# Kernel optimization log

Hardware: AMD Instinct MI355X
Metric: run time of the kernel (lower is better)

The kernel has to match this reference:

```python
import jax, jax.numpy as jnp
import numpy as np

N_NODES = 50000
N_EDGES = 800000
D = 128          # node / edge / u feature dim
OUT = 128
N_GRAPHS = 64
IN1 = 4 * D      # 512
IN2 = D + OUT + D  # 384


def setup_inputs() -> dict:
    key = jax.random.key(0)
    ks = jax.random.split(key, 10)
    x = jax.random.normal(ks[0], (N_NODES, D), dtype=jnp.float32)
    edge_index = jax.random.randint(ks[1], (2, N_EDGES), 0, N_NODES, dtype=jnp.int64)
    edge_attr = jax.random.normal(ks[2], (N_EDGES, D), dtype=jnp.float32)
    u = jax.random.normal(ks[3], (N_GRAPHS, D), dtype=jnp.float32)
    batch = jnp.sort(jax.random.randint(ks[4], (N_NODES,), 0, N_GRAPHS, dtype=jnp.int64))
    # MLP params (Linear: y = x @ W.T + b), kaiming-ish scale
    W1 = jax.random.normal(ks[5], (OUT, IN1), dtype=jnp.float32) / np.sqrt(IN1)
    b1 = jnp.zeros((OUT,), dtype=jnp.float32)
    W2 = jax.random.normal(ks[6], (OUT, IN2), dtype=jnp.float32) / np.sqrt(IN2)
    b2 = jnp.zeros((OUT,), dtype=jnp.float32)
    return {"x": x, "edge_index": edge_index, "edge_attr": edge_attr,
            "u": u, "batch": batch, "W1": W1, "b1": b1, "W2": W2, "b2": b2}


def reference(x, edge_index, edge_attr, u, batch, W1, b1, W2, b2):
    src, dst = edge_index[0], edge_index[1]
    source_features = x[src]                  # [E, D]
    dest_features = x[dst]                    # [E, D]
    u_edge = u[batch[dst]]                    # [E, D]
    edge_input = jnp.concatenate([dest_features, source_features, edge_attr, u_edge], axis=1)  # [E, IN1]
    edge_messages = jax.nn.relu(edge_input @ W1.T + b1)  # [E, OUT]
    aggregated = jax.ops.segment_sum(edge_messages, dst, num_segments=x.shape[0])  # [N, OUT]
    u_expanded = u[batch]                     # [N, D]
    node_input = jnp.concatenate([x, aggregated, u_expanded], axis=1)  # [N, IN2]
    return jax.nn.relu(node_input @ W2.T + b2)  # [N, OUT]
```

## Files before the change

kernel.cpp:

```cpp
#include <hip/hip_runtime.h>
#include <stdint.h>

#define NNODES 50000
#define NEDGES 800000
#define DIM 128
#define IN1 512
#define IN2 384
#define NSB 196

typedef __attribute__((ext_vector_type(8))) short bf16x8;
typedef __attribute__((ext_vector_type(8))) unsigned short u16x8;
typedef __attribute__((ext_vector_type(4))) float f32x4;
typedef __attribute__((ext_vector_type(4))) uint32_t u32x4;

__device__ __forceinline__ unsigned short f2bf(float f) {
  union { float f; uint32_t u; } v; v.f = f;
  return (unsigned short)((v.u + 0x7FFFu + ((v.u >> 16) & 1u)) >> 16);
}
__device__ __forceinline__ float bf2f(unsigned short u) {
  union { uint32_t u; float f; } v; v.u = ((uint32_t)u) << 16;
  return v.f;
}
__device__ __forceinline__ uint32_t cvtpk(float lo, float hi) {
  uint32_t r;
  asm volatile("v_cvt_pk_bf16_f32 %0, %1, %2" : "=v"(r) : "v"(lo), "v"(hi));
  return r;
}

__device__ __forceinline__ void cvt8(const float* __restrict__ p, unsigned short* dst, int sidx) {
  float4 f0 = *(const float4*)(p);
  float4 f1 = *(const float4*)(p + 4);
  u16x8 o;
  o[0] = f2bf(f0.x); o[1] = f2bf(f0.y); o[2] = f2bf(f0.z); o[3] = f2bf(f0.w);
  o[4] = f2bf(f1.x); o[5] = f2bf(f1.y); o[6] = f2bf(f1.z); o[7] = f2bf(f1.w);
  *(u16x8*)(dst + sidx) = o;
}

__device__ __forceinline__ void mfma128(const unsigned short* As, const unsigned short* Bs,
                                        f32x4 acc[4][4], int wm, int wn, int l) {
#pragma unroll
  for (int kk = 0; kk < 4; ++kk) {
    bf16x8 a[4], b[4];
#pragma unroll
    for (int mi = 0; mi < 4; ++mi) {
      int row = wm * 64 + mi * 16 + (l & 15);
      int idx = (row * 128 + kk * 32 + (l >> 4) * 8) ^ ((row & 7) << 3);
      a[mi] = *(const bf16x8*)(As + idx);
    }
#pragma unroll
    for (int ni = 0; ni < 4; ++ni) {
      int nrow = wn * 64 + ni * 16 + (l & 15);
      int idx = (nrow * 128 + kk * 32 + (l >> 4) * 8) ^ ((nrow & 7) << 3);
      b[ni] = *(const bf16x8*)(Bs + idx);
    }
#pragma unroll
    for (int mi = 0; mi < 4; ++mi)
#pragma unroll
      for (int ni = 0; ni < 4; ++ni)
        acc[mi][ni] = __builtin_amdgcn_mfma_f32_16x16x32_bf16(a[mi], b[ni], acc[mi][ni], 0, 0, 0);
  }
}

__global__ void p0_kernel(const float* __restrict__ u,
                          const float* __restrict__ W1, const float* __restrict__ b1,
                          const float* __restrict__ W2, const float* __restrict__ b2,
                          float* __restrict__ Ud, float* __restrict__ Uc) {
  int g = blockIdx.x, c = threadIdx.x;
  const float* ur = u + (size_t)g * DIM;
  const float* w1 = W1 + (size_t)c * IN1 + 384;
  const float* w2 = W2 + (size_t)c * IN2 + 256;
  float s1 = b1[c], s2 = b2[c];
  for (int k = 0; k < DIM; ++k) { float uv = ur[k]; s1 += uv * w1[k]; s2 += uv * w2[k]; }
  Ud[g * DIM + c] = s1;
  Uc[g * DIM + c] = s2;
}

__global__ void wconv_kernel(const float* __restrict__ W1, const float* __restrict__ W2,
                             unsigned short* __restrict__ Wt) {
  int t = blockIdx.x * 256 + threadIdx.x;
  int tile = t >> 14, rem = t & 16383, n = rem >> 7, k = rem & 127;
  float v = (tile < 3) ? W1[(size_t)n * IN1 + tile * 128 + k]
                       : W2[(size_t)n * IN2 + (tile - 3) * 128 + k];
  int lin = ((n * 128 + (k & ~7)) ^ ((n & 7) << 3)) | (k & 7);
  Wt[tile * 16384 + lin] = f2bf(v);
}

__global__ __launch_bounds__(256, 2) void p1_kernel(
    const float* __restrict__ x, const int* __restrict__ batch,
    const unsigned short* __restrict__ Wt,
    const float* __restrict__ Ud, const float* __restrict__ Uc,
    unsigned short* __restrict__ Xad, unsigned short* __restrict__ Xb,
    unsigned short* __restrict__ Yx) {
  __shared__ __align__(16) unsigned short As[128 * 128];
  __shared__ __align__(16) unsigned short Bs[128 * 128];
  const int t = threadIdx.x, l = t & 63, w = t >> 6, wm = w >> 1, wn = w & 1;
  const int n0 = blockIdx.x * 128, r = t >> 1, h = t & 1;
  const int swz = (r & 7) << 3;
  {
    int n = n0 + r; if (n >= NNODES) n = NNODES - 1;
    const float* rowp = x + (size_t)n * DIM + h * 64;
#pragma unroll
    for (int i = 0; i < 8; ++i) cvt8(rowp + i * 8, As, (r * 128 + h * 64 + i * 8) ^ swz);
  }
#pragma unroll
  for (int p = 0; p < 3; ++p) {
    __syncthreads();
    {
      const u16x8* wsrc = (const u16x8*)(Wt + (size_t)((p == 2) ? 3 : p) * 16384);
      u16x8* bdst = (u16x8*)Bs;
#pragma unroll
      for (int i = 0; i < 8; ++i) bdst[t + i * 256] = wsrc[t + i * 256];
    }
    __syncthreads();
    f32x4 acc[4][4] = {};
    mfma128(As, Bs, acc, wm, wn, l);
#pragma unroll
    for (int mi = 0; mi < 4; ++mi)
#pragma unroll
      for (int rr = 0; rr < 4; ++rr) {
        int m = wm * 64 + mi * 16 + (l >> 4) * 4 + rr;
        int n = n0 + m;
        if (n < NNODES) {
          int g = batch[n];
#pragma unroll
          for (int ni = 0; ni < 4; ++ni) {
            int col = wn * 64 + ni * 16 + (l & 15);
            float v = acc[mi][ni][rr];
            if (p == 0)      Xad[(size_t)n * DIM + col] = f2bf(v + Ud[g * DIM + col]);
            else if (p == 1) Xb [(size_t)n * DIM + col] = f2bf(v);
            else             Yx [(size_t)n * DIM + col] = f2bf(v + Uc[g * DIM + col]);
          }
        }
      }
  }
}

__global__ void hist_kernel(const int* __restrict__ dstI, int* __restrict__ count) {
  int e = blockIdx.x * 256 + threadIdx.x;
  if (e < NEDGES) atomicAdd(&count[dstI[e]], 1);
}

__global__ void scan1_kernel(const int* __restrict__ count, int* __restrict__ bsum) {
  __shared__ int ws[4];
  int i = blockIdx.x * 256 + threadIdx.x;
  int v = (i < NNODES) ? count[i] : 0;
  int l = threadIdx.x & 63;
#pragma unroll
  for (int off = 32; off > 0; off >>= 1) v += __shfl_down(v, off);
  if (l == 0) ws[threadIdx.x >> 6] = v;
  __syncthreads();
  if (threadIdx.x == 0) bsum[blockIdx.x] = ws[0] + ws[1] + ws[2] + ws[3];
}

__global__ void scan2_kernel(const int* __restrict__ bsum, int* __restrict__ bpre) {
  __shared__ int s[256];
  int i = threadIdx.x;
  int v = (i < NSB) ? bsum[i] : 0;
  s[i] = v; __syncthreads();
  for (int off = 1; off < 256; off <<= 1) {
    int u = (i >= off) ? s[i - off] : 0;
    __syncthreads();
    s[i] += u;
    __syncthreads();
  }
  if (i < NSB) bpre[i] = s[i] - v;
}

__global__ void scan3_kernel(const int* __restrict__ count, const int* __restrict__ bpre,
                             int* __restrict__ rowptr) {
  __shared__ int s[256];
  int b = blockIdx.x, i = threadIdx.x, g = b * 256 + i;
  int v = (g < NNODES) ? count[g] : 0;
  s[i] = v; __syncthreads();
  for (int off = 1; off < 256; off <<= 1) {
    int u = (i >= off) ? s[i - off] : 0;
    __syncthreads();
    s[i] += u;
    __syncthreads();
  }
  if (g < NNODES) rowptr[g] = bpre[b] + s[i] - v;
}

__global__ void scatter_kernel(const int* __restrict__ srcI, const int* __restrict__ dstI,
                               int* __restrict__ rowptr, uint64_t* __restrict__ esd) {
  int e = blockIdx.x * 256 + threadIdx.x;
  if (e < NEDGES) {
    int d = dstI[e], s = srcI[e];
    int pos = atomicAdd(&rowptr[d], 1);
    esd[pos] = ((uint64_t)(uint32_t)e << 32) | ((uint32_t)s << 16) | (uint32_t)d;
  }
}

__global__ __launch_bounds__(512, 6) void edge2_kernel(
    const float* __restrict__ ea, const uint64_t* __restrict__ esd,
    const unsigned short* __restrict__ W1cs,
    const unsigned short* __restrict__ Xad, const unsigned short* __restrict__ Xb,
    float* __restrict__ agg) {
  __shared__ __align__(16) unsigned short smem[24576];
  __shared__ int dlds[64];
  __shared__ int slds[64];
  unsigned short* As = smem;
  unsigned short* Bs = smem + 8192;
  unsigned short* Xbs = smem;
  float* Ms = (float*)(smem + 8192);

  const int t = threadIdx.x, l = t & 63, w = t >> 6;
  const int wm = w >> 2, wn = w & 3;
  int bid = blockIdx.x;
  const int nwg = NEDGES / 64, q = nwg >> 3, r8 = nwg & 7;
  int xcd = bid & 7, off = bid >> 3;
  int wg = (xcd < r8) ? xcd * (q + 1) + off : r8 * (q + 1) + (xcd - r8) * q + off;
  const int p0 = wg * 64;
  const int r = t >> 3, o = t & 7;

  {
    const u16x8* wsrc = (const u16x8*)W1cs;
    u16x8* bdst = (u16x8*)Bs;
#pragma unroll
    for (int i = 0; i < 4; ++i) bdst[t + i * 512] = wsrc[t + i * 512];
  }
  if (t < 64) {
    uint64_t v = esd[p0 + t];
    dlds[t] = (int)(v & 0xFFFF);
    slds[t] = (int)((v >> 16) & 0xFFFF);
  }
  {
    uint64_t v = esd[p0 + r];
    int e = (int)(v >> 32);
    const float* rowp = ea + (size_t)e * DIM + o * 16;
    float4 f0 = *(const float4*)(rowp);
    float4 f1 = *(const float4*)(rowp + 4);
    float4 f2 = *(const float4*)(rowp + 8);
    float4 f3 = *(const float4*)(rowp + 12);
    const int swz = (r & 7) << 3;
    u32x4 g0 = {cvtpk(f0.x, f0.y), cvtpk(f0.z, f0.w), cvtpk(f1.x, f1.y), cvtpk(f1.z, f1.w)};
    u32x4 g1 = {cvtpk(f2.x, f2.y), cvtpk(f2.z, f2.w), cvtpk(f3.x, f3.y), cvtpk(f3.z, f3.w)};
    *(u32x4*)(As + ((r * 128 + o * 16) ^ swz)) = g0;
    *(u32x4*)(As + ((r * 128 + o * 16 + 8) ^ swz)) = g1;
  }
  __syncthreads();

  f32x4 acc[2][2] = {};
#pragma unroll
  for (int kk = 0; kk < 4; ++kk) {
    bf16x8 a[2], b[2];
#pragma unroll
    for (int mi = 0; mi < 2; ++mi) {
      int row = wm * 32 + mi * 16 + (l & 15);
      int idx = (row * 128 + kk * 32 + (l >> 4) * 8) ^ ((row & 7) << 3);
      a[mi] = *(const bf16x8*)(As + idx);
    }
#pragma unroll
    for (int ni = 0; ni < 2; ++ni) {
      int n = wn * 32 + ni * 16 + (l & 15);
      int idx = (n * 128 + kk * 32 + (l >> 4) * 8) ^ ((n & 7) << 3);
      b[ni] = *(const bf16x8*)(Bs + idx);
    }
#pragma unroll
    for (int mi = 0; mi < 2; ++mi)
#pragma unroll
      for (int ni = 0; ni < 2; ++ni)
        acc[mi][ni] = __builtin_amdgcn_mfma_f32_16x16x32_bf16(a[mi], b[ni], acc[mi][ni], 0, 0, 0);
  }
  __syncthreads();

  {
    int sm = slds[r];
    const u16x8* xr = (const u16x8*)(Xb + (size_t)sm * DIM);
    int sw = ((r >> 2) & 3) << 1;
    u16x8 xv0 = xr[o * 2];
    u16x8 xv1 = xr[o * 2 + 1];
    u16x8* xb8 = (u16x8*)Xbs;
    xb8[r * 16 + ((o * 2) ^ sw)] = xv0;
    xb8[r * 16 + ((o * 2 + 1) ^ sw)] = xv1;
  }
  __syncthreads();

#pragma unroll
  for (int mi = 0; mi < 2; ++mi)
#pragma unroll
    for (int rr = 0; rr < 4; ++rr) {
      int m = wm * 32 + mi * 16 + (l >> 4) * 4 + rr;
      int d = dlds[m];
      const unsigned short* xa = Xad + (size_t)d * DIM;
      int cs = ((m >> 2) & 3) << 3;
      int cx = ((m >> 2) & 3) << 4;
#pragma unroll
      for (int ni = 0; ni < 2; ++ni) {
        int col = wn * 32 + ni * 16 + (l & 15);
        float v = acc[mi][ni][rr] + bf2f(xa[col]) + bf2f(Xbs[m * 128 + (col ^ cx)]);
        Ms[m * 128 + (col ^ cs)] = fmaxf(v, 0.0f);
      }
    }
  __syncthreads();

  {
    int col = t & 127, row0 = (t >> 7) * 16;
    float sum = 0.0f;
    int curd = -1;
    for (int i = 0; i < 16; ++i) {
      int rowi = row0 + i;
      int d = dlds[rowi];
      float v = Ms[rowi * 128 + (col ^ (((rowi >> 2) & 3) << 3))];
      if (d != curd) {
        if (curd >= 0) unsafeAtomicAdd(agg + (size_t)curd * DIM + col, sum);
        curd = d; sum = v;
      } else {
        sum += v;
      }
    }
    if (curd >= 0) unsafeAtomicAdd(agg + (size_t)curd * DIM + col, sum);
  }
}

__global__ __launch_bounds__(256, 2) void edge_kernel(
    const float* __restrict__ ea, const int* __restrict__ srcI, const int* __restrict__ dstI,
    const unsigned short* __restrict__ W1cs,
    const unsigned short* __restrict__ Xad, const unsigned short* __restrict__ Xb,
    float* __restrict__ agg) {
  __shared__ __align__(16) unsigned short As[128 * 128];
  __shared__ __align__(16) unsigned short Bs[128 * 128];
  const int t = threadIdx.x, l = t & 63, w = t >> 6, wm = w >> 1, wn = w & 1;
  const int e0 = blockIdx.x * 128, r = t >> 1, h = t & 1;
  const int swz = (r & 7) << 3;
  {
    const float* rowp = ea + (size_t)(e0 + r) * DIM + h * 64;
#pragma unroll
    for (int i = 0; i < 8; ++i) cvt8(rowp + i * 8, As, (r * 128 + h * 64 + i * 8) ^ swz);
  }
  {
    const u16x8* wsrc = (const u16x8*)W1cs;
    u16x8* bdst = (u16x8*)Bs;
#pragma unroll
    for (int i = 0; i < 8; ++i) bdst[t + i * 256] = wsrc[t + i * 256];
  }
  __syncthreads();
  f32x4 acc[4][4] = {};
  mfma128(As, Bs, acc, wm, wn, l);
#pragma unroll
  for (int mi = 0; mi < 4; ++mi)
#pragma unroll
    for (int rr = 0; rr < 4; ++rr) {
      int m = wm * 64 + mi * 16 + (l >> 4) * 4 + rr;
      int e = e0 + m;
      int d = dstI[e], s = srcI[e];
      const unsigned short* xa = Xad + (size_t)d * DIM;
      const unsigned short* xb = Xb + (size_t)s * DIM;
      float* ag = agg + (size_t)d * DIM;
#pragma unroll
      for (int ni = 0; ni < 4; ++ni) {
        int col = wn * 64 + ni * 16 + (l & 15);
        float v = acc[mi][ni][rr] + bf2f(xa[col]) + bf2f(xb[col]);
        unsafeAtomicAdd(ag + col, fmaxf(v, 0.0f));
      }
    }
}

__global__ __launch_bounds__(256, 2) void node_kernel(
    const float* __restrict__ agg, const unsigned short* __restrict__ Wt,
    const unsigned short* __restrict__ Yx, float* __restrict__ out) {
  __shared__ __align__(16) unsigned short As[128 * 128];
  __shared__ __align__(16) unsigned short Bs[128 * 128];
  const int t = threadIdx.x, l = t & 63, w = t >> 6, wm = w >> 1, wn = w & 1;
  const int n0 = blockIdx.x * 128, r = t >> 1, h = t & 1;
  const int swz = (r & 7) << 3;
  {
    int n = n0 + r; if (n >= NNODES) n = NNODES - 1;
    const float* rowp = agg + (size_t)n * DIM + h * 64;
#pragma unroll
    for (int i = 0; i < 8; ++i) cvt8(rowp + i * 8, As, (r * 128 + h * 64 + i * 8) ^ swz);
  }
  {
    const u16x8* wsrc = (const u16x8*)(Wt + (size_t)4 * 16384);
    u16x8* bdst = (u16x8*)Bs;
#pragma unroll
    for (int i = 0; i < 8; ++i) bdst[t + i * 256] = wsrc[t + i * 256];
  }
  __syncthreads();
  f32x4 acc[4][4] = {};
  mfma128(As, Bs, acc, wm, wn, l);
#pragma unroll
  for (int mi = 0; mi < 4; ++mi)
#pragma unroll
    for (int rr = 0; rr < 4; ++rr) {
      int m = wm * 64 + mi * 16 + (l >> 4) * 4 + rr;
      int n = n0 + m;
      if (n < NNODES) {
        float* orow = out + (size_t)n * DIM;
#pragma unroll
        for (int ni = 0; ni < 4; ++ni) {
          int col = wn * 64 + ni * 16 + (l & 15);
          float v = acc[mi][ni][rr] + bf2f(Yx[(size_t)n * DIM + col]);
          orow[col] = fmaxf(v, 0.0f);
        }
      }
    }
}

extern "C" void kernel_launch(void* const* d_in, const int* in_sizes, int n_in,
                              void* d_out, int out_size, void* d_ws, size_t ws_size,
                              hipStream_t stream) {
  const float* x   = (const float*)d_in[0];
  const int* ei    = (const int*)d_in[1];
  const float* ea  = (const float*)d_in[2];
  const float* u   = (const float*)d_in[3];
  const int* batch = (const int*)d_in[4];
  const float* W1  = (const float*)d_in[5];
  const float* b1  = (const float*)d_in[6];
  const float* W2  = (const float*)d_in[7];
  const float* b2  = (const float*)d_in[8];
  float* out = (float*)d_out;
  const int* srcI = ei;
  const int* dstI = ei + NEDGES;

  const size_t XAD_B = (size_t)NNODES * DIM * 2;
  const size_t U_B   = (size_t)64 * DIM * 4;
  const size_t WT_B  = (size_t)5 * 16384 * 2;
  const size_t ESD_B = (size_t)NEDGES * 8;
  const size_t CNT_B = (size_t)(NNODES + 64) * 4;
  const size_t BS_B  = 4096;
  const size_t need_base = 3 * XAD_B + 2 * U_B + WT_B;
  const size_t need_sort = need_base + ESD_B + 2 * CNT_B + 2 * BS_B;

  char* p = (char*)d_ws;
  unsigned short* Xad = (unsigned short*)p; p += XAD_B;
  unsigned short* Xb  = (unsigned short*)p; p += XAD_B;
  unsigned short* Yx  = (unsigned short*)p; p += XAD_B;
  float* Ud = (float*)p; p += U_B;
  float* Uc = (float*)p; p += U_B;
  unsigned short* Wt = (unsigned short*)p; p += WT_B;
  uint64_t* esd = (uint64_t*)p; p += ESD_B;
  int* count  = (int*)p; p += CNT_B;
  int* rowptr = (int*)p; p += CNT_B;
  int* bsum = (int*)p; p += BS_B;
  int* bpre = (int*)p;

  float* agg = out;

  if (ws_size >= need_sort) {
    hipMemsetAsync(agg, 0, (size_t)NNODES * DIM * sizeof(float), stream);
    hipMemsetAsync(count, 0, CNT_B, stream);
    hist_kernel<<<(NEDGES + 255) / 256, 256, 0, stream>>>(dstI, count);
    scan1_kernel<<<NSB, 256, 0, stream>>>(count, bsum);
    scan2_kernel<<<1, 256, 0, stream>>>(bsum, bpre);
    scan3_kernel<<<NSB, 256, 0, stream>>>(count, bpre, rowptr);
    scatter_kernel<<<(NEDGES + 255) / 256, 256, 0, stream>>>(srcI, dstI, rowptr, esd);
    p0_kernel<<<64, 128, 0, stream>>>(u, W1, b1, W2, b2, Ud, Uc);
    wconv_kernel<<<320, 256, 0, stream>>>(W1, W2, Wt);
    p1_kernel<<<(NNODES + 127) / 128, 256, 0, stream>>>(x, batch, Wt, Ud, Uc, Xad, Xb, Yx);
    edge2_kernel<<<NEDGES / 64, 512, 0, stream>>>(ea, esd, Wt + 2 * 16384, Xad, Xb, agg);
    node_kernel<<<(NNODES + 127) / 128, 256, 0, stream>>>(agg, Wt, Yx, out);
  } else if (ws_size >= need_base) {
    hipMemsetAsync(agg, 0, (size_t)NNODES * DIM * sizeof(float), stream);
    p0_kernel<<<64, 128, 0, stream>>>(u, W1, b1, W2, b2, Ud, Uc);
    wconv_kernel<<<320, 256, 0, stream>>>(W1, W2, Wt);
    p1_kernel<<<(NNODES + 127) / 128, 256, 0, stream>>>(x, batch, Wt, Ud, Uc, Xad, Xb, Yx);
    edge_kernel<<<NEDGES / 128, 256, 0, stream>>>(ea, srcI, dstI, Wt + 2 * 16384, Xad, Xb, agg);
    node_kernel<<<(NNODES + 127) / 128, 256, 0, stream>>>(agg, Wt, Yx, out);
  }
}
```

Before: 309.8 us.

## Keep W1 edge-attr tile in registers, shrink edge LDS, fuse setup kernels

The edge kernel now loads its slice of the bf16 W1 edge-attribute weights straight into registers instead of staging them in shared memory. It stores the post-ReLU message tile as bf16 rather than fp32, which cuts LDS from 48KB to 32KB and raises launch bounds to 8 blocks per CU. The source-row gather is moved before the first barrier so it overlaps with the MFMA setup. On the host side, two memsets are merged into one zero kernel and the p0/wconv kernels into one launch to reduce launch overhead. Rounding messages to bf16 before the segment sum adds precision loss, and the extra register use may limit occupancy.

```diff
diff --git a/kernel.cpp b/kernel.cpp
--- a/kernel.cpp
+++ b/kernel.cpp
@@ -61,28 +61,37 @@
   }
 }
 
-__global__ void p0_kernel(const float* __restrict__ u,
-                          const float* __restrict__ W1, const float* __restrict__ b1,
-                          const float* __restrict__ W2, const float* __restrict__ b2,
-                          float* __restrict__ Ud, float* __restrict__ Uc) {
-  int g = blockIdx.x, c = threadIdx.x;
-  const float* ur = u + (size_t)g * DIM;
-  const float* w1 = W1 + (size_t)c * IN1 + 384;
-  const float* w2 = W2 + (size_t)c * IN2 + 256;
-  float s1 = b1[c], s2 = b2[c];
-  for (int k = 0; k < DIM; ++k) { float uv = ur[k]; s1 += uv * w1[k]; s2 += uv * w2[k]; }
-  Ud[g * DIM + c] = s1;
-  Uc[g * DIM + c] = s2;
-}
-
-__global__ void wconv_kernel(const float* __restrict__ W1, const float* __restrict__ W2,
-                             unsigned short* __restrict__ Wt) {
-  int t = blockIdx.x * 256 + threadIdx.x;
-  int tile = t >> 14, rem = t & 16383, n = rem >> 7, k = rem & 127;
-  float v = (tile < 3) ? W1[(size_t)n * IN1 + tile * 128 + k]
-                       : W2[(size_t)n * IN2 + (tile - 3) * 128 + k];
-  int lin = ((n * 128 + (k & ~7)) ^ ((n & 7) << 3)) | (k & 7);
-  Wt[tile * 16384 + lin] = f2bf(v);
+__global__ void zero_kernel(float4* __restrict__ a, int n4, int* __restrict__ c, int nc) {
+  int i = blockIdx.x * 256 + threadIdx.x;
+  int stride = gridDim.x * 256;
+  for (int k = i; k < n4; k += stride) a[k] = float4{0.f, 0.f, 0.f, 0.f};
+  for (int k = i; k < nc; k += stride) c[k] = 0;
+}
+
+__global__ void wconv_p0_kernel(const float* __restrict__ W1, const float* __restrict__ W2,
+                                const float* __restrict__ u, const float* __restrict__ b1,
+                                const float* __restrict__ b2,
+                                unsigned short* __restrict__ Wt,
+                                float* __restrict__ Ud, float* __restrict__ Uc) {
+  int b = blockIdx.x;
+  if (b < 320) {
+    int t = b * 256 + threadIdx.x;
+    int tile = t >> 14, rem = t & 16383, n = rem >> 7, k = rem & 127;
+    float v = (tile < 3) ? W1[(size_t)n * IN1 + tile * 128 + k]
+                         : W2[(size_t)n * IN2 + (tile - 3) * 128 + k];
+    int lin = ((n * 128 + (k & ~7)) ^ ((n & 7) << 3)) | (k & 7);
+    Wt[tile * 16384 + lin] = f2bf(v);
+  } else {
+    int g = (b - 320) * 2 + (threadIdx.x >> 7);
+    int c = threadIdx.x & 127;
+    const float* ur = u + (size_t)g * DIM;
+    const float* w1 = W1 + (size_t)c * IN1 + 384;
+    const float* w2 = W2 + (size_t)c * IN2 + 256;
+    float s1 = b1[c], s2 = b2[c];
+    for (int k = 0; k < DIM; ++k) { float uv = ur[k]; s1 += uv * w1[k]; s2 += uv * w2[k]; }
+    Ud[g * DIM + c] = s1;
+    Uc[g * DIM + c] = s2;
+  }
 }
 
 __global__ __launch_bounds__(256, 2) void p1_kernel(
@@ -191,18 +200,16 @@
   }
 }
 
-__global__ __launch_bounds__(512, 6) void edge2_kernel(
+__global__ __launch_bounds__(512, 8) void edge2_kernel(
     const float* __restrict__ ea, const uint64_t* __restrict__ esd,
     const unsigned short* __restrict__ W1cs,
     const unsigned short* __restrict__ Xad, const unsigned short* __restrict__ Xb,
     float* __restrict__ agg) {
-  __shared__ __align__(16) unsigned short smem[24576];
+  __shared__ __align__(16) unsigned short smem[16384];
   __shared__ int dlds[64];
-  __shared__ int slds[64];
-  unsigned short* As = smem;
-  unsigned short* Bs = smem + 8192;
-  unsigned short* Xbs = smem;
-  float* Ms = (float*)(smem + 8192);
+  unsigned short* As  = smem;
+  unsigned short* Xbs = smem + 8192;
+  unsigned short* Ms  = smem;
 
   const int t = threadIdx.x, l = t & 63, w = t >> 6;
   const int wm = w >> 2, wn = w & 3;
@@ -213,19 +220,19 @@
   const int p0 = wg * 64;
   const int r = t >> 3, o = t & 7;
 
-  {
-    const u16x8* wsrc = (const u16x8*)W1cs;
-    u16x8* bdst = (u16x8*)Bs;
-#pragma unroll
-    for (int i = 0; i < 4; ++i) bdst[t + i * 512] = wsrc[t + i * 512];
-  }
-  if (t < 64) {
-    uint64_t v = esd[p0 + t];
-    dlds[t] = (int)(v & 0xFFFF);
-    slds[t] = (int)((v >> 16) & 0xFFFF);
-  }
-  {
-    uint64_t v = esd[p0 + r];
+  bf16x8 bfr[2][4];
+#pragma unroll
+  for (int kk = 0; kk < 4; ++kk)
+#pragma unroll
+    for (int ni = 0; ni < 2; ++ni) {
+      int n = wn * 32 + ni * 16 + (l & 15);
+      int idx = (n * 128 + kk * 32 + (l >> 4) * 8) ^ ((n & 7) << 3);
+      bfr[ni][kk] = *(const bf16x8*)(W1cs + idx);
+    }
+
+  uint64_t v = esd[p0 + r];
+  if (t < 64) dlds[t] = (int)(esd[p0 + t] & 0xFFFF);
+  {
     int e = (int)(v >> 32);
     const float* rowp = ea + (size_t)e * DIM + o * 16;
     float4 f0 = *(const float4*)(rowp);
@@ -238,35 +245,9 @@
     *(u32x4*)(As + ((r * 128 + o * 16) ^ swz)) = g0;
     *(u32x4*)(As + ((r * 128 + o * 16 + 8) ^ swz)) = g1;
   }
-  __syncthreads();
-
-  f32x4 acc[2][2] = {};
-#pragma unroll
-  for (int kk = 0; kk < 4; ++kk) {
-    bf16x8 a[2], b[2];
-#pragma unroll
-    for (int mi = 0; mi < 2; ++mi) {
-      int row = wm * 32 + mi * 16 + (l & 15);
-      int idx = (row * 128 + kk * 32 + (l >> 4) * 8) ^ ((row & 7) << 3);
-      a[mi] = *(const bf16x8*)(As + idx);
-    }
-#pragma unroll
-    for (int ni = 0; ni < 2; ++ni) {
-      int n = wn * 32 + ni * 16 + (l & 15);
-      int idx = (n * 128 + kk * 32 + (l >> 4) * 8) ^ ((n & 7) << 3);
-      b[ni] = *(const bf16x8*)(Bs + idx);
-    }
-#pragma unroll
-    for (int mi = 0; mi < 2; ++mi)
-#pragma unroll
-      for (int ni = 0; ni < 2; ++ni)
-        acc[mi][ni] = __builtin_amdgcn_mfma_f32_16x16x32_bf16(a[mi], b[ni], acc[mi][ni], 0, 0, 0);
-  }
-  __syncthreads();
-
-  {
-    int sm = slds[r];
-    const u16x8* xr = (const u16x8*)(Xb + (size_t)sm * DIM);
+  {
+    int s = (int)((v >> 16) & 0xFFFF);
+    const u16x8* xr = (const u16x8*)(Xb + (size_t)s * DIM);
     int sw = ((r >> 2) & 3) << 1;
     u16x8 xv0 = xr[o * 2];
     u16x8 xv1 = xr[o * 2 + 1];
@@ -276,6 +257,24 @@
   }
   __syncthreads();
 
+  f32x4 acc[2][2] = {};
+#pragma unroll 2
+  for (int kk = 0; kk < 4; ++kk) {
+    bf16x8 a[2];
+#pragma unroll
+    for (int mi = 0; mi < 2; ++mi) {
+      int row = wm * 32 + mi * 16 + (l & 15);
+      int idx = (row * 128 + kk * 32 + (l >> 4) * 8) ^ ((row & 7) << 3);
+      a[mi] = *(const bf16x8*)(As + idx);
+    }
+#pragma unroll
+    for (int mi = 0; mi < 2; ++mi)
+#pragma unroll
+      for (int ni = 0; ni < 2; ++ni)
+        acc[mi][ni] = __builtin_amdgcn_mfma_f32_16x16x32_bf16(a[mi], bfr[ni][kk], acc[mi][ni], 0, 0, 0);
+  }
+  __syncthreads();
+
 #pragma unroll
   for (int mi = 0; mi < 2; ++mi)
 #pragma unroll
@@ -283,13 +282,12 @@
       int m = wm * 32 + mi * 16 + (l >> 4) * 4 + rr;
       int d = dlds[m];
       const unsigned short* xa = Xad + (size_t)d * DIM;
-      int cs = ((m >> 2) & 3) << 3;
       int cx = ((m >> 2) & 3) << 4;
 #pragma unroll
       for (int ni = 0; ni < 2; ++ni) {
         int col = wn * 32 + ni * 16 + (l & 15);
-        float v = acc[mi][ni][rr] + bf2f(xa[col]) + bf2f(Xbs[m * 128 + (col ^ cx)]);
-        Ms[m * 128 + (col ^ cs)] = fmaxf(v, 0.0f);
+        float vv = acc[mi][ni][rr] + bf2f(xa[col]) + bf2f(Xbs[m * 128 + (col ^ cx)]);
+        Ms[m * 128 + (col ^ cx)] = f2bf(fmaxf(vv, 0.0f));
       }
     }
   __syncthreads();
@@ -301,12 +299,12 @@
     for (int i = 0; i < 16; ++i) {
       int rowi = row0 + i;
       int d = dlds[rowi];
-      float v = Ms[rowi * 128 + (col ^ (((rowi >> 2) & 3) << 3))];
+      float vv = bf2f(Ms[rowi * 128 + (col ^ (((rowi >> 2) & 3) << 4))]);
       if (d != curd) {
         if (curd >= 0) unsafeAtomicAdd(agg + (size_t)curd * DIM + col, sum);
-        curd = d; sum = v;
+        curd = d; sum = vv;
       } else {
-        sum += v;
+        sum += vv;
       }
     }
     if (curd >= 0) unsafeAtomicAdd(agg + (size_t)curd * DIM + col, sum);
@@ -436,24 +434,22 @@
   int* bpre = (int*)p;
 
   float* agg = out;
+  const int nAgg4 = NNODES * DIM / 4;
 
   if (ws_size >= need_sort) {
-    hipMemsetAsync(agg, 0, (size_t)NNODES * DIM * sizeof(float), stream);
-    hipMemsetAsync(count, 0, CNT_B, stream);
+    zero_kernel<<<2048, 256, 0, stream>>>((float4*)agg, nAgg4, count, NNODES + 64);
     hist_kernel<<<(NEDGES + 255) / 256, 256, 0, stream>>>(dstI, count);
     scan1_kernel<<<NSB, 256, 0, stream>>>(count, bsum);
     scan2_kernel<<<1, 256, 0, stream>>>(bsum, bpre);
     scan3_kernel<<<NSB, 256, 0, stream>>>(count, bpre, rowptr);
     scatter_kernel<<<(NEDGES + 255) / 256, 256, 0, stream>>>(srcI, dstI, rowptr, esd);
-    p0_kernel<<<64, 128, 0, stream>>>(u, W1, b1, W2, b2, Ud, Uc);
-    wconv_kernel<<<320, 256, 0, stream>>>(W1, W2, Wt);
+    wconv_p0_kernel<<<352, 256, 0, stream>>>(W1, W2, u, b1, b2, Wt, Ud, Uc);
     p1_kernel<<<(NNODES + 127) / 128, 256, 0, stream>>>(x, batch, Wt, Ud, Uc, Xad, Xb, Yx);
     edge2_kernel<<<NEDGES / 64, 512, 0, stream>>>(ea, esd, Wt + 2 * 16384, Xad, Xb, agg);
     node_kernel<<<(NNODES + 127) / 128, 256, 0, stream>>>(agg, Wt, Yx, out);
   } else if (ws_size >= need_base) {
-    hipMemsetAsync(agg, 0, (size_t)NNODES * DIM * sizeof(float), stream);
-    p0_kernel<<<64, 128, 0, stream>>>(u, W1, b1, W2, b2, Ud, Uc);
-    wconv_kernel<<<320, 256, 0, stream>>>(W1, W2, Wt);
+    zero_kernel<<<2048, 256, 0, stream>>>((float4*)agg, nAgg4, (int*)Ud, 0);
+    wconv_p0_kernel<<<352, 256, 0, stream>>>(W1, W2, u, b1, b2, Wt, Ud, Uc);
     p1_kernel<<<(NNODES + 127) / 128, 256, 0, stream>>>(x, batch, Wt, Ud, Uc, Xad, Xb, Yx);
     edge_kernel<<<NEDGES / 128, 256, 0, stream>>>(ea, srcI, dstI, Wt + 2 * 16384, Xad, Xb, agg);
     node_kernel<<<(NNODES + 127) / 128, 256, 0, stream>>>(agg, Wt, Yx, out);
```

Measured after the change: 627.5 us. 2.03x slower.
